# Kernel tuning notes

Hardware: AMD Instinct MI355X
Metric: run time of the kernel (lower is better)

## Reference

```python
import jax, jax.numpy as jnp
import numpy as np

BOARD = 19
TOKENS = BOARD * BOARD          # 361
C = 512
H = 8
DH = C // H                     # 64
MLP = 2048
SPAN = 2 * BOARD - 1            # 37
TABLE = SPAN * SPAN             # 1369
EPS = 1e-6


def _relative_position_index(board_size):
    coords = np.arange(board_size, dtype=np.int32)
    row, col = np.meshgrid(coords, coords, indexing='ij')
    flat = np.stack((row.reshape(-1), col.reshape(-1)), axis=1)
    rel = flat[:, None, :] - flat[None, :, :]
    span = 2 * board_size - 1
    return (rel[..., 0] + board_size - 1) * span + (rel[..., 1] + board_size - 1)


REL_INDEX = jnp.asarray(_relative_position_index(BOARD))  # [T, T] int32


def _layernorm(x, scale, bias):
    mu = jnp.mean(x, axis=-1, keepdims=True)
    var = jnp.mean(jnp.square(x - mu), axis=-1, keepdims=True)
    return (x - mu) * jax.lax.rsqrt(var + EPS) * scale + bias


def setup_inputs() -> dict:
    key = jax.random.key(0)
    ks = jax.random.split(key, 12)
    B = 256
    s = lambda k, shape, sc: jax.random.normal(k, shape, dtype=jnp.float32) * sc
    return {
        'x': s(ks[0], (B, TOKENS, C), 1.0),
        'ln1_scale': jnp.ones((C,), jnp.float32),
        'ln1_bias': jnp.zeros((C,), jnp.float32),
        'Wq': s(ks[1], (C, H, DH), C ** -0.5),
        'bq': jnp.zeros((H, DH), jnp.float32),
        'Wk': s(ks[2], (C, H, DH), C ** -0.5),
        'bk': jnp.zeros((H, DH), jnp.float32),
        'Wv': s(ks[3], (C, H, DH), C ** -0.5),
        'bv': jnp.zeros((H, DH), jnp.float32),
        'Wo': s(ks[4], (C, C), C ** -0.5),
        'bo': jnp.zeros((C,), jnp.float32),
        'rel_pos_bias': s(ks[5], (H, TABLE), 0.02),
        'ln2_scale': jnp.ones((C,), jnp.float32),
        'ln2_bias': jnp.zeros((C,), jnp.float32),
        'W1': s(ks[6], (C, MLP), C ** -0.5),
        'b1': jnp.zeros((MLP,), jnp.float32),
        'W2': s(ks[7], (MLP, C), MLP ** -0.5),
        'b2': jnp.zeros((C,), jnp.float32),
    }


def reference(x, ln1_scale, ln1_bias, Wq, bq, Wk, bk, Wv, bv, Wo, bo,
              rel_pos_bias, ln2_scale, ln2_bias, W1, b1, W2, b2):
    # --- attention ---
    y = _layernorm(x, ln1_scale, ln1_bias)
    q = jnp.einsum('btc,chd->bthd', y, Wq) + bq
    k = jnp.einsum('btc,chd->bthd', y, Wk) + bk
    v = jnp.einsum('btc,chd->bthd', y, Wv) + bv
    logits = jnp.einsum('bthd,bshd->bhts', q, k) * jnp.float32(DH ** -0.5)
    rel_bias = jnp.take(rel_pos_bias, REL_INDEX.reshape(-1), axis=1)
    rel_bias = rel_bias.reshape(H, TOKENS, TOKENS)          # [H, T, T]
    logits = logits + rel_bias[None]
    attn = jax.nn.softmax(logits.astype(jnp.float32), axis=-1).astype(x.dtype)
    ctx = jnp.einsum('bhts,bshd->bthd', attn, v)
    ctx = ctx.reshape(ctx.shape[0], ctx.shape[1], C)
    x = x + ctx @ Wo + bo
    # --- MLP ---
    y = _layernorm(x, ln2_scale, ln2_bias)
    y = jax.nn.gelu(y @ W1 + b1, approximate=True)
    return x + y @ W2 + b2
```

## Files before the change

kernel.cpp:

```cpp
#include <hip/hip_runtime.h>
#include <hip/hip_bf16.h>

#define TOKENS 361
#define CDIM 512
#define NHEAD 8
#define DHEAD 64
#define MLPDIM 2048
#define BATCH 256
#define NTOK (BATCH * TOKENS)
#define HTOK (NTOK / 2)
#define SPAN 37
#define QKVSTR 1536

typedef unsigned int uint32;

typedef __attribute__((ext_vector_type(8))) short bf16x8;
typedef __attribute__((ext_vector_type(4))) float f32x4;

__device__ __forceinline__ unsigned short f2bfu(float f) {
  union { float f; uint32 i; } c; c.f = f;
  uint32 i = c.i;
  uint32 r = (i + 0x7fffu + ((i >> 16) & 1u)) >> 16;
  return (unsigned short)r;
}
__device__ __forceinline__ float bfu2f(unsigned short u) {
  union { uint32 i; float f; } c; c.i = ((uint32)u) << 16; return c.f;
}
__device__ __forceinline__ float lo2f(uint32 u) {
  union { uint32 i; float f; } c; c.i = u << 16; return c.f;
}
__device__ __forceinline__ float hi2f(uint32 u) {
  union { uint32 i; float f; } c; c.i = u & 0xffff0000u; return c.f;
}

__device__ __forceinline__ void gload16(const void* g, void* l) {
  __builtin_amdgcn_global_load_lds((const __attribute__((address_space(1))) void*)g,
                                   (__attribute__((address_space(3))) void*)l, 16, 0, 0);
}

__global__ __launch_bounds__(256) void transpose_conv(
    const float* __restrict__ in, unsigned short* __restrict__ out, int R, int Cc) {
  __shared__ float tile[32][33];
  int c0 = blockIdx.x * 32, r0 = blockIdx.y * 32;
  int tx = threadIdx.x & 31, ty = threadIdx.x >> 5;
#pragma unroll
  for (int i = 0; i < 32; i += 8)
    tile[ty + i][tx] = in[(size_t)(r0 + ty + i) * Cc + c0 + tx];
  __syncthreads();
#pragma unroll
  for (int i = 0; i < 32; i += 8)
    out[(size_t)(c0 + ty + i) * R + r0 + tx] = f2bfu(tile[tx][ty + i]);
}

__global__ __launch_bounds__(256) void concat_bias(
    const float* __restrict__ a, const float* __restrict__ b,
    const float* __restrict__ c, float* __restrict__ o) {
  int i = blockIdx.x * 256 + threadIdx.x;
  o[i] = i < 512 ? a[i] : (i < 1024 ? b[i - 512] : c[i - 1024]);
}

__global__ __launch_bounds__(256) void ln_f32(
    const float* __restrict__ x, const float* __restrict__ sc,
    const float* __restrict__ bs, unsigned short* __restrict__ y) {
  int token = blockIdx.x * 4 + (threadIdx.x >> 6);
  int lane = threadIdx.x & 63;
  const float4* xp = (const float4*)(x + (size_t)token * CDIM + lane * 8);
  float4 f0 = xp[0], f1 = xp[1];
  float v[8] = {f0.x, f0.y, f0.z, f0.w, f1.x, f1.y, f1.z, f1.w};
  float sum = 0.f, sumsq = 0.f;
#pragma unroll
  for (int j = 0; j < 8; ++j) { sum += v[j]; sumsq += v[j] * v[j]; }
#pragma unroll
  for (int off = 1; off < 64; off <<= 1) {
    sum += __shfl_xor(sum, off);
    sumsq += __shfl_xor(sumsq, off);
  }
  float mu = sum * (1.f / 512.f);
  float var = sumsq * (1.f / 512.f) - mu * mu;
  float rs = rsqrtf(var + 1e-6f);
  const float4* sp = (const float4*)(sc + lane * 8);
  const float4* bp = (const float4*)(bs + lane * 8);
  float4 s0 = sp[0], s1 = sp[1], b0 = bp[0], b1 = bp[1];
  float sv[8] = {s0.x, s0.y, s0.z, s0.w, s1.x, s1.y, s1.z, s1.w};
  float bv[8] = {b0.x, b0.y, b0.z, b0.w, b1.x, b1.y, b1.z, b1.w};
  uint32 ov[4];
#pragma unroll
  for (int j = 0; j < 4; ++j) {
    float o0 = (v[2 * j] - mu) * rs * sv[2 * j] + bv[2 * j];
    float o1 = (v[2 * j + 1] - mu) * rs * sv[2 * j + 1] + bv[2 * j + 1];
    ov[j] = (uint32)f2bfu(o0) | ((uint32)f2bfu(o1) << 16);
  }
  uint4 outv = {ov[0], ov[1], ov[2], ov[3]};
  *(uint4*)(y + (size_t)token * CDIM + lane * 8) = outv;
}

__global__ __launch_bounds__(256) void ln_bf16(
    const unsigned short* __restrict__ x, const float* __restrict__ sc,
    const float* __restrict__ bs, unsigned short* __restrict__ y) {
  int token = blockIdx.x * 4 + (threadIdx.x >> 6);
  int lane = threadIdx.x & 63;
  uint4 pk = *(const uint4*)(x + (size_t)token * CDIM + lane * 8);
  uint32 uu[4] = {pk.x, pk.y, pk.z, pk.w};
  float v[8];
#pragma unroll
  for (int j = 0; j < 4; ++j) { v[2 * j] = lo2f(uu[j]); v[2 * j + 1] = hi2f(uu[j]); }
  float sum = 0.f, sumsq = 0.f;
#pragma unroll
  for (int j = 0; j < 8; ++j) { sum += v[j]; sumsq += v[j] * v[j]; }
#pragma unroll
  for (int off = 1; off < 64; off <<= 1) {
    sum += __shfl_xor(sum, off);
    sumsq += __shfl_xor(sumsq, off);
  }
  float mu = sum * (1.f / 512.f);
  float var = sumsq * (1.f / 512.f) - mu * mu;
  float rs = rsqrtf(var + 1e-6f);
  const float4* sp = (const float4*)(sc + lane * 8);
  const float4* bp = (const float4*)(bs + lane * 8);
  float4 s0 = sp[0], s1 = sp[1], b0 = bp[0], b1 = bp[1];
  float sv[8] = {s0.x, s0.y, s0.z, s0.w, s1.x, s1.y, s1.z, s1.w};
  float bv[8] = {b0.x, b0.y, b0.z, b0.w, b1.x, b1.y, b1.z, b1.w};
  uint32 ov[4];
#pragma unroll
  for (int j = 0; j < 4; ++j) {
    float o0 = (v[2 * j] - mu) * rs * sv[2 * j] + bv[2 * j];
    float o1 = (v[2 * j + 1] - mu) * rs * sv[2 * j + 1] + bv[2 * j + 1];
    ov[j] = (uint32)f2bfu(o0) | ((uint32)f2bfu(o1) << 16);
  }
  uint4 outv = {ov[0], ov[1], ov[2], ov[3]};
  *(uint4*)(y + (size_t)token * CDIM + lane * 8) = outv;
}

__device__ __forceinline__ float gelu_tanh(float u) {
  float c2 = 0.7978845608028654f * (u + 0.044715f * u * u * u);
  float e = __expf(2.f * c2);
  float th = 1.f - 2.f / (e + 1.f);
  return 0.5f * u * (1.f + th);
}

template <int EPI>
__global__ __launch_bounds__(256) void gemm_bt(
    const unsigned short* __restrict__ A, const unsigned short* __restrict__ BT,
    const float* __restrict__ bias, const float* __restrict__ resf,
    const unsigned short* __restrict__ resb, void* __restrict__ Cc,
    int M, int N, int K, int nbx) {
  __shared__ unsigned short SH[16384];
  int tid = threadIdx.x;
  int wave = tid >> 6, lane = tid & 63;
  int quad = lane >> 4, l16 = lane & 15;

  int nwg = gridDim.x, bid = blockIdx.x;
  int qq = nwg >> 3, rr = nwg & 7;
  int xcd = bid & 7, loc = bid >> 3;
  int L = (xcd < rr ? xcd * (qq + 1) : rr * (qq + 1) + (xcd - rr) * qq) + loc;
  int m0 = (L / nbx) * 128, n0 = (L % nbx) * 128;
  int wm = (wave >> 1) * 64, wn = (wave & 1) * 64;

  f32x4 acc[4][4];
#pragma unroll
  for (int i = 0; i < 4; ++i)
#pragma unroll
    for (int j = 0; j < 4; ++j) acc[i][j] = (f32x4){0.f, 0.f, 0.f, 0.f};

  int srow = tid >> 2;
  int schunk = ((tid & 3) ^ ((tid >> 3) & 3)) * 8;
  const unsigned short* gA = A + (size_t)(m0 + srow) * K + schunk;
  const unsigned short* gA2 = gA + (size_t)64 * K;
  const unsigned short* gB = BT + (size_t)(n0 + srow) * K + schunk;
  const unsigned short* gB2 = gB + (size_t)64 * K;

  {
    unsigned short* a = SH;
    unsigned short* bS = SH + 8192;
    gload16(gA, a + wave * 512);
    gload16(gA2, a + 2048 + wave * 512);
    gload16(gB, bS + wave * 512);
    gload16(gB2, bS + 2048 + wave * 512);
  }
  __syncthreads();

  int rq = (quad ^ ((l16 >> 1) & 3)) * 8;
  int cur = 0;
  for (int k0 = 0; k0 < K; k0 += 32) {
    if (k0 + 32 < K) {
      int nb = cur ^ 1;
      unsigned short* a = SH + nb * 4096;
      unsigned short* bS = SH + 8192 + nb * 4096;
      gload16(gA + k0 + 32, a + wave * 512);
      gload16(gA2 + k0 + 32, a + 2048 + wave * 512);
      gload16(gB + k0 + 32, bS + wave * 512);
      gload16(gB2 + k0 + 32, bS + 2048 + wave * 512);
    }
    const unsigned short* As = SH + cur * 4096;
    const unsigned short* Bs = SH + 8192 + cur * 4096;
    bf16x8 af[4], bfr[4];
#pragma unroll
    for (int mi = 0; mi < 4; ++mi)
      af[mi] = *(const bf16x8*)&As[(wm + mi * 16 + l16) * 32 + rq];
#pragma unroll
    for (int ni = 0; ni < 4; ++ni)
      bfr[ni] = *(const bf16x8*)&Bs[(wn + ni * 16 + l16) * 32 + rq];
#pragma unroll
    for (int mi = 0; mi < 4; ++mi)
#pragma unroll
      for (int ni = 0; ni < 4; ++ni)
        acc[mi][ni] = __builtin_amdgcn_mfma_f32_16x16x32_bf16(af[mi], bfr[ni], acc[mi][ni], 0, 0, 0);
    __syncthreads();
    cur ^= 1;
  }

  unsigned short* o16 = (unsigned short*)Cc;
  float* o32 = (float*)Cc;
  if (EPI == 3) {
#pragma unroll
    for (int ni = 0; ni < 4; ++ni) {
      int gc = n0 + wn + ni * 16 + l16;
      float bz = bias[gc];
#pragma unroll
      for (int mi = 0; mi < 4; ++mi) {
#pragma unroll
        for (int r = 0; r < 4; ++r) {
          int gr = m0 + wm + mi * 16 + quad * 4 + r;
          float val = acc[mi][ni][r] + bz;
          val += bfu2f(resb[(size_t)gr * N + gc]);
          o32[(size_t)gr * N + gc] = val;
        }
      }
    }
  } else {
#pragma unroll
    for (int ni = 0; ni < 4; ++ni) {
      int gc = n0 + wn + ni * 16 + l16;
      float bz = bias[gc];
#pragma unroll
      for (int mi = 0; mi < 4; ++mi) {
#pragma unroll
        for (int r = 0; r < 4; ++r) {
          int lr = wm + mi * 16 + quad * 4 + r;
          float val = acc[mi][ni][r] + bz;
          if (EPI == 1) val = gelu_tanh(val);
          if (EPI == 2) val += resf[(size_t)(m0 + lr) * N + gc];
          SH[lr * 128 + wn + ni * 16 + l16] = f2bfu(val);
        }
      }
    }
    __syncthreads();
    int tg = tid >> 4, t15 = tid & 15;
#pragma unroll
    for (int j = 0; j < 8; ++j) {
      int row = j * 16 + tg;
      uint4 w = *(const uint4*)&SH[row * 128 + t15 * 8];
      *(uint4*)(o16 + (size_t)(m0 + row) * N + n0 + t15 * 8) = w;
    }
  }
}

#define SROW 72
#define PSTR 392
__global__ __launch_bounds__(256, 1) void attn_mfma(
    const unsigned short* __restrict__ qkv, const float* __restrict__ relb,
    unsigned short* __restrict__ ctx) {
  __shared__ unsigned short Ks[368 * SROW];
  __shared__ unsigned short VT[64 * PSTR];
  __shared__ unsigned short Ps[64 * PSTR];
  __shared__ float biasF[1369];
  int b = blockIdx.x >> 3, h = blockIdx.x & 7;
  int tid = threadIdx.x;
  int wave = tid >> 6, lane = tid & 63;
  int quad = lane >> 4, l16 = lane & 15;
  size_t baseq = ((size_t)b * TOKENS) * QKVSTR + h * DHEAD;
  size_t basec = ((size_t)b * TOKENS) * CDIM + h * DHEAD;
  const unsigned short* kp = qkv + baseq + 512;
  const unsigned short* vp = qkv + baseq + 1024;

  for (int vv = tid; vv < TOKENS * 8; vv += 256) {
    int r = vv >> 3, c = (vv & 7) * 8;
    *(uint4*)&Ks[r * SROW + c] = *(const uint4*)(kp + (size_t)r * QKVSTR + c);
  }
  if (tid < 56) {
    int r = 361 + (tid >> 3), c = (tid & 7) * 8;
    *(uint4*)&Ks[r * SROW + c] = (uint4){0u, 0u, 0u, 0u};
  }
  for (int vv = tid; vv < TOKENS * 8; vv += 256) {
    int s = vv >> 3, c = (vv & 7) * 8;
    uint4 pk = *(const uint4*)(vp + (size_t)s * QKVSTR + c);
    unsigned short* dst = &VT[c * PSTR + s];
    uint32 w0 = pk.x, w1 = pk.y, w2 = pk.z, w3 = pk.w;
    dst[0]        = (unsigned short)w0;  dst[PSTR]     = (unsigned short)(w0 >> 16);
    dst[2 * PSTR] = (unsigned short)w1;  dst[3 * PSTR] = (unsigned short)(w1 >> 16);
    dst[4 * PSTR] = (unsigned short)w2;  dst[5 * PSTR] = (unsigned short)(w2 >> 16);
    dst[6 * PSTR] = (unsigned short)w3;  dst[7 * PSTR] = (unsigned short)(w3 >> 16);
  }
  for (int vv = tid; vv < 64 * 23; vv += 256) {
    int s = 361 + (vv >> 6), d = vv & 63;
    VT[d * PSTR + s] = 0;
  }
  for (int i = tid; i < 1369; i += 256) biasF[i] = relb[h * 1369 + i];
  for (int i = lane; i < 256; i += 64) {
    int rrp = i >> 4, cc = i & 15;
    Ps[(wave * 16 + rrp) * PSTR + 368 + cc] = 0;
  }
  __syncthreads();

  for (int t0 = 0; t0 < TOKENS; t0 += 64) {
    int rowb = t0 + wave * 16;
    const unsigned short* qrow = qkv + baseq + (size_t)(rowb + l16) * QKVSTR + quad * 8;
    bf16x8 aq0 = *(const bf16x8*)(qrow);
    bf16x8 aq1 = *(const bf16x8*)(qrow + 32);
    int tb[4];
#pragma unroll
    for (int r = 0; r < 4; ++r) {
      int t = rowb + quad * 4 + r;
      if (t > 360) t = 360;
      int rt = t / 19, ct = t - rt * 19;
      tb[r] = rt * SPAN + ct + (18 * SPAN + 18);
    }
    f32x4 sc[23];
#pragma unroll
    for (int n = 0; n < 23; ++n) {
      const unsigned short* kr = &Ks[(n * 16 + l16) * SROW + quad * 8];
      bf16x8 b0 = *(const bf16x8*)kr;
      bf16x8 b1 = *(const bf16x8*)(kr + 32);
      f32x4 a = {0.f, 0.f, 0.f, 0.f};
      a = __builtin_amdgcn_mfma_f32_16x16x32_bf16(aq0, b0, a, 0, 0, 0);
      a = __builtin_amdgcn_mfma_f32_16x16x32_bf16(aq1, b1, a, 0, 0, 0);
      sc[n] = a;
    }
    float mx[4] = {-1e30f, -1e30f, -1e30f, -1e30f};
#pragma unroll
    for (int n = 0; n < 23; ++n) {
      int s = n * 16 + l16;
      int sv = s > 360 ? 360 : s;
      int rs = sv / 19, cs = sv - rs * 19;
      int sb = rs * SPAN + cs;
#pragma unroll
      for (int r = 0; r < 4; ++r) {
        float val = sc[n][r] * 0.125f + biasF[tb[r] - sb];
        if (s > 360) val = -1e30f;
        sc[n][r] = val;
        mx[r] = fmaxf(mx[r], val);
      }
    }
#pragma unroll
    for (int off = 1; off < 16; off <<= 1)
#pragma unroll
      for (int r = 0; r < 4; ++r) mx[r] = fmaxf(mx[r], __shfl_xor(mx[r], off));
    float sm[4] = {0.f, 0.f, 0.f, 0.f};
#pragma unroll
    for (int n = 0; n < 23; ++n)
#pragma unroll
      for (int r = 0; r < 4; ++r) {
        float p = __expf(sc[n][r] - mx[r]);
        sc[n][r] = p;
        sm[r] += p;
      }
#pragma unroll
    for (int off = 1; off < 16; off <<= 1)
#pragma unroll
      for (int r = 0; r < 4; ++r) sm[r] += __shfl_xor(sm[r], off);
    float inv[4];
#pragma unroll
    for (int r = 0; r < 4; ++r) inv[r] = 1.f / sm[r];
#pragma unroll
    for (int n = 0; n < 23; ++n)
#pragma unroll
      for (int r = 0; r < 4; ++r)
        Ps[(wave * 16 + quad * 4 + r) * PSTR + n * 16 + l16] = f2bfu(sc[n][r] * inv[r]);
    f32x4 pacc[4];
#pragma unroll
    for (int ni = 0; ni < 4; ++ni) pacc[ni] = (f32x4){0.f, 0.f, 0.f, 0.f};
#pragma unroll
    for (int kk = 0; kk < 12; ++kk) {
      bf16x8 pa = *(const bf16x8*)&Ps[(wave * 16 + l16) * PSTR + kk * 32 + quad * 8];
#pragma unroll
      for (int ni = 0; ni < 4; ++ni) {
        bf16x8 vb = *(const bf16x8*)&VT[(ni * 16 + l16) * PSTR + kk * 32 + quad * 8];
        pacc[ni] = __builtin_amdgcn_mfma_f32_16x16x32_bf16(pa, vb, pacc[ni], 0, 0, 0);
      }
    }
#pragma unroll
    for (int ni = 0; ni < 4; ++ni)
#pragma unroll
      for (int r = 0; r < 4; ++r) {
        int t = rowb + quad * 4 + r;
        if (t < TOKENS)
          ctx[basec + (size_t)t * CDIM + ni * 16 + l16] = f2bfu(pacc[ni][r]);
      }
  }
}

extern "C" void kernel_launch(void* const* d_in, const int* in_sizes, int n_in,
                              void* d_out, int out_size, void* d_ws, size_t ws_size,
                              hipStream_t stream) {
  const float* x     = (const float*)d_in[0];
  const float* ln1_s = (const float*)d_in[1];
  const float* ln1_b = (const float*)d_in[2];
  const float* Wq    = (const float*)d_in[3];
  const float* bq    = (const float*)d_in[4];
  const float* Wk    = (const float*)d_in[5];
  const float* bk    = (const float*)d_in[6];
  const float* Wv    = (const float*)d_in[7];
  const float* bv    = (const float*)d_in[8];
  const float* Wo    = (const float*)d_in[9];
  const float* bo    = (const float*)d_in[10];
  const float* relb  = (const float*)d_in[11];
  const float* ln2_s = (const float*)d_in[12];
  const float* ln2_b = (const float*)d_in[13];
  const float* W1    = (const float*)d_in[14];
  const float* b1    = (const float*)d_in[15];
  const float* W2    = (const float*)d_in[16];
  const float* b2    = (const float*)d_in[17];
  float* out = (float*)d_out;

  char* ws = (char*)d_ws;
  unsigned short* WqT = (unsigned short*)ws;
  unsigned short* WkT = WqT + 512 * 512;
  unsigned short* WvT = WkT + 512 * 512;
  unsigned short* WoT = WvT + 512 * 512;
  unsigned short* W1T = WoT + 512 * 512;
  unsigned short* W2T = W1T + 512 * 2048;
  float* bqkv = (float*)(W2T + 2048 * 512);
  unsigned short* yb  = (unsigned short*)(bqkv + 1536);
  unsigned short* x1b = yb + (size_t)NTOK * CDIM;
  unsigned short* qkvb = x1b + (size_t)NTOK * CDIM;
  unsigned short* ctxb = qkvb + (size_t)HTOK * QKVSTR;
  unsigned short* hdn  = qkvb;

  dim3 blk(256);
  transpose_conv<<<dim3(16, 16), blk, 0, stream>>>(Wq, WqT, 512, 512);
  transpose_conv<<<dim3(16, 16), blk, 0, stream>>>(Wk, WkT, 512, 512);
  transpose_conv<<<dim3(16, 16), blk, 0, stream>>>(Wv, WvT, 512, 512);
  transpose_conv<<<dim3(16, 16), blk, 0, stream>>>(Wo, WoT, 512, 512);
  transpose_conv<<<dim3(64, 16), blk, 0, stream>>>(W1, W1T, 512, 2048);
  transpose_conv<<<dim3(16, 64), blk, 0, stream>>>(W2, W2T, 2048, 512);
  concat_bias<<<dim3(6), blk, 0, stream>>>(bq, bk, bv, bqkv);

  ln_f32<<<NTOK / 4, blk, 0, stream>>>(x, ln1_s, ln1_b, yb);

  for (int c = 0; c < 2; ++c) {
    size_t off = (size_t)c * HTOK;
    const unsigned short* yc = yb + off * CDIM;
    gemm_bt<0><<<dim3(361 * 12), blk, 0, stream>>>(yc, WqT, bqkv, nullptr, nullptr,
                                                   qkvb, HTOK, 1536, 512, 12);
    attn_mfma<<<dim3((BATCH / 2) * NHEAD), blk, 0, stream>>>(qkvb, relb, ctxb);
    gemm_bt<2><<<dim3(361 * 4), blk, 0, stream>>>(ctxb, WoT, bo, x + off * CDIM, nullptr,
                                                  x1b + off * CDIM, HTOK, 512, 512, 4);
  }

  ln_bf16<<<NTOK / 4, blk, 0, stream>>>(x1b, ln2_s, ln2_b, yb);

  for (int c = 0; c < 2; ++c) {
    size_t off = (size_t)c * HTOK;
    gemm_bt<1><<<dim3(361 * 16), blk, 0, stream>>>(yb + off * CDIM, W1T, b1, nullptr, nullptr,
                                                   hdn, HTOK, 2048, 512, 16);
    gemm_bt<3><<<dim3(361 * 4), blk, 0, stream>>>(hdn, W2T, b2, nullptr, x1b + off * CDIM,
                                                  out + off * CDIM, HTOK, 512, 2048, 4);
  }
}
```

Before: 1.717 ms.

## Swizzle attention LDS layouts, widen to 8 waves, stage EPI3 epilogue through LDS

The attention kernel now runs 512 threads (8 waves), so each block covers 128 query rows per iteration, three iterations in total. K, V-transpose and P are stored in LDS with XOR swizzles instead of padded strides, which is meant to avoid bank conflicts. P is written and consumed in three chunks so the LDS buffer for it is smaller, and s_setprio is raised around the MFMA loops. Separately, the fp32 residual epilogue of the GEMM is staged through shared memory in two halves so the residual reads and fp32 output writes become vectorized and coalesced. The cost is extra barriers in that epilogue and more register pressure in the wider attention block.

```diff
diff --git a/kernel.cpp b/kernel.cpp
--- a/kernel.cpp
+++ b/kernel.cpp
@@ -212,19 +212,35 @@
   unsigned short* o16 = (unsigned short*)Cc;
   float* o32 = (float*)Cc;
   if (EPI == 3) {
-#pragma unroll
-    for (int ni = 0; ni < 4; ++ni) {
-      int gc = n0 + wn + ni * 16 + l16;
-      float bz = bias[gc];
-#pragma unroll
-      for (int mi = 0; mi < 4; ++mi) {
-#pragma unroll
-        for (int r = 0; r < 4; ++r) {
-          int gr = m0 + wm + mi * 16 + quad * 4 + r;
-          float val = acc[mi][ni][r] + bz;
-          val += bfu2f(resb[(size_t)gr * N + gc]);
-          o32[(size_t)gr * N + gc] = val;
+    float* SHf = (float*)SH;
+#pragma unroll
+    for (int h2 = 0; h2 < 2; ++h2) {
+      __syncthreads();
+      if ((wn >> 6) == h2) {
+#pragma unroll
+        for (int ni = 0; ni < 4; ++ni) {
+          float bz = bias[n0 + h2 * 64 + ni * 16 + l16];
+#pragma unroll
+          for (int mi = 0; mi < 4; ++mi) {
+#pragma unroll
+            for (int r = 0; r < 4; ++r) {
+              int row = wm + mi * 16 + quad * 4 + r;
+              SHf[row * 64 + ni * 16 + l16] = acc[mi][ni][r] + bz;
+            }
+          }
         }
+      }
+      __syncthreads();
+#pragma unroll
+      for (int j = 0; j < 8; ++j) {
+        int idx = j * 256 + tid;
+        int row = idx >> 4, c4 = (idx & 15) * 4;
+        size_t goff = (size_t)(m0 + row) * N + n0 + h2 * 64 + c4;
+        uint2 rb = *(const uint2*)(resb + goff);
+        float4 sv = *(const float4*)&SHf[row * 64 + c4];
+        sv.x += lo2f(rb.x); sv.y += hi2f(rb.x);
+        sv.z += lo2f(rb.y); sv.w += hi2f(rb.y);
+        *(float4*)(o32 + goff) = sv;
       }
     }
   } else {
@@ -255,55 +271,53 @@
   }
 }
 
-#define SROW 72
-#define PSTR 392
-__global__ __launch_bounds__(256, 1) void attn_mfma(
+#define KROW 64
+#define VROW 384
+#define PROW 128
+__global__ __launch_bounds__(512, 1) void attn_mfma(
     const unsigned short* __restrict__ qkv, const float* __restrict__ relb,
     unsigned short* __restrict__ ctx) {
-  __shared__ unsigned short Ks[368 * SROW];
-  __shared__ unsigned short VT[64 * PSTR];
-  __shared__ unsigned short Ps[64 * PSTR];
+  __shared__ unsigned short Ks[384 * KROW];
+  __shared__ unsigned short VT[64 * VROW];
+  __shared__ unsigned short Ps[128 * PROW];
   __shared__ float biasF[1369];
   int b = blockIdx.x >> 3, h = blockIdx.x & 7;
   int tid = threadIdx.x;
   int wave = tid >> 6, lane = tid & 63;
   int quad = lane >> 4, l16 = lane & 15;
+  int l8 = l16 & 7;
   size_t baseq = ((size_t)b * TOKENS) * QKVSTR + h * DHEAD;
   size_t basec = ((size_t)b * TOKENS) * CDIM + h * DHEAD;
   const unsigned short* kp = qkv + baseq + 512;
   const unsigned short* vp = qkv + baseq + 1024;
 
-  for (int vv = tid; vv < TOKENS * 8; vv += 256) {
-    int r = vv >> 3, c = (vv & 7) * 8;
-    *(uint4*)&Ks[r * SROW + c] = *(const uint4*)(kp + (size_t)r * QKVSTR + c);
-  }
-  if (tid < 56) {
-    int r = 361 + (tid >> 3), c = (tid & 7) * 8;
-    *(uint4*)&Ks[r * SROW + c] = (uint4){0u, 0u, 0u, 0u};
-  }
-  for (int vv = tid; vv < TOKENS * 8; vv += 256) {
+  for (int vv = tid; vv < 384 * 8; vv += 512) {
+    int r = vv >> 3, c8 = vv & 7;
+    uint4 val = (uint4){0u, 0u, 0u, 0u};
+    if (r < TOKENS) val = *(const uint4*)(kp + (size_t)r * QKVSTR + c8 * 8);
+    *(uint4*)&Ks[r * KROW + ((c8 ^ (r & 7)) << 3)] = val;
+  }
+  for (int vv = tid; vv < TOKENS * 8; vv += 512) {
     int s = vv >> 3, c = (vv & 7) * 8;
     uint4 pk = *(const uint4*)(vp + (size_t)s * QKVSTR + c);
-    unsigned short* dst = &VT[c * PSTR + s];
-    uint32 w0 = pk.x, w1 = pk.y, w2 = pk.z, w3 = pk.w;
-    dst[0]        = (unsigned short)w0;  dst[PSTR]     = (unsigned short)(w0 >> 16);
-    dst[2 * PSTR] = (unsigned short)w1;  dst[3 * PSTR] = (unsigned short)(w1 >> 16);
-    dst[4 * PSTR] = (unsigned short)w2;  dst[5 * PSTR] = (unsigned short)(w2 >> 16);
-    dst[6 * PSTR] = (unsigned short)w3;  dst[7 * PSTR] = (unsigned short)(w3 >> 16);
-  }
-  for (int vv = tid; vv < 64 * 23; vv += 256) {
+    uint32 w[4] = {pk.x, pk.y, pk.z, pk.w};
+    int g0 = s >> 3, s7 = s & 7;
+#pragma unroll
+    for (int j = 0; j < 8; ++j) {
+      unsigned short hv = (unsigned short)(w[j >> 1] >> ((j & 1) * 16));
+      int d0 = c + j;
+      VT[d0 * VROW + ((g0 ^ (d0 & 7)) << 3) + s7] = hv;
+    }
+  }
+  for (int vv = tid; vv < 64 * 23; vv += 512) {
     int s = 361 + (vv >> 6), d = vv & 63;
-    VT[d * PSTR + s] = 0;
-  }
-  for (int i = tid; i < 1369; i += 256) biasF[i] = relb[h * 1369 + i];
-  for (int i = lane; i < 256; i += 64) {
-    int rrp = i >> 4, cc = i & 15;
-    Ps[(wave * 16 + rrp) * PSTR + 368 + cc] = 0;
-  }
+    VT[d * VROW + (((s >> 3) ^ (d & 7)) << 3) + (s & 7)] = 0;
+  }
+  for (int i = tid; i < 1369; i += 512) biasF[i] = relb[h * 1369 + i];
   __syncthreads();
 
-  for (int t0 = 0; t0 < TOKENS; t0 += 64) {
-    int rowb = t0 + wave * 16;
+  for (int it = 0; it < 3; ++it) {
+    int rowb = it * 128 + wave * 16;
     const unsigned short* qrow = qkv + baseq + (size_t)(rowb + l16) * QKVSTR + quad * 8;
     bf16x8 aq0 = *(const bf16x8*)(qrow);
     bf16x8 aq1 = *(const bf16x8*)(qrow + 32);
@@ -315,20 +329,22 @@
       int rt = t / 19, ct = t - rt * 19;
       tb[r] = rt * SPAN + ct + (18 * SPAN + 18);
     }
-    f32x4 sc[23];
-#pragma unroll
-    for (int n = 0; n < 23; ++n) {
-      const unsigned short* kr = &Ks[(n * 16 + l16) * SROW + quad * 8];
-      bf16x8 b0 = *(const bf16x8*)kr;
-      bf16x8 b1 = *(const bf16x8*)(kr + 32);
+    f32x4 sc[24];
+    __builtin_amdgcn_s_setprio(1);
+#pragma unroll
+    for (int n = 0; n < 24; ++n) {
+      const unsigned short* kr = &Ks[(n * 16 + l16) * KROW];
+      bf16x8 b0 = *(const bf16x8*)(kr + ((quad ^ l8) << 3));
+      bf16x8 b1 = *(const bf16x8*)(kr + (((quad + 4) ^ l8) << 3));
       f32x4 a = {0.f, 0.f, 0.f, 0.f};
       a = __builtin_amdgcn_mfma_f32_16x16x32_bf16(aq0, b0, a, 0, 0, 0);
       a = __builtin_amdgcn_mfma_f32_16x16x32_bf16(aq1, b1, a, 0, 0, 0);
       sc[n] = a;
     }
+    __builtin_amdgcn_s_setprio(0);
     float mx[4] = {-1e30f, -1e30f, -1e30f, -1e30f};
 #pragma unroll
-    for (int n = 0; n < 23; ++n) {
+    for (int n = 0; n < 24; ++n) {
       int s = n * 16 + l16;
       int sv = s > 360 ? 360 : s;
       int rs = sv / 19, cs = sv - rs * 19;
@@ -347,7 +363,7 @@
       for (int r = 0; r < 4; ++r) mx[r] = fmaxf(mx[r], __shfl_xor(mx[r], off));
     float sm[4] = {0.f, 0.f, 0.f, 0.f};
 #pragma unroll
-    for (int n = 0; n < 23; ++n)
+    for (int n = 0; n < 24; ++n)
 #pragma unroll
       for (int r = 0; r < 4; ++r) {
         float p = __expf(sc[n][r] - mx[r]);
@@ -361,22 +377,34 @@
     float inv[4];
 #pragma unroll
     for (int r = 0; r < 4; ++r) inv[r] = 1.f / sm[r];
-#pragma unroll
-    for (int n = 0; n < 23; ++n)
-#pragma unroll
-      for (int r = 0; r < 4; ++r)
-        Ps[(wave * 16 + quad * 4 + r) * PSTR + n * 16 + l16] = f2bfu(sc[n][r] * inv[r]);
     f32x4 pacc[4];
 #pragma unroll
     for (int ni = 0; ni < 4; ++ni) pacc[ni] = (f32x4){0.f, 0.f, 0.f, 0.f};
 #pragma unroll
-    for (int kk = 0; kk < 12; ++kk) {
-      bf16x8 pa = *(const bf16x8*)&Ps[(wave * 16 + l16) * PSTR + kk * 32 + quad * 8];
-#pragma unroll
-      for (int ni = 0; ni < 4; ++ni) {
-        bf16x8 vb = *(const bf16x8*)&VT[(ni * 16 + l16) * PSTR + kk * 32 + quad * 8];
-        pacc[ni] = __builtin_amdgcn_mfma_f32_16x16x32_bf16(pa, vb, pacc[ni], 0, 0, 0);
-      }
+    for (int ch = 0; ch < 3; ++ch) {
+#pragma unroll
+      for (int nl = 0; nl < 8; ++nl) {
+        int n = ch * 8 + nl;
+#pragma unroll
+        for (int r = 0; r < 4; ++r) {
+          int prow = wave * 16 + quad * 4 + r;
+          int g = ((nl << 1) + (l16 >> 3)) ^ ((quad * 4 + r) & 7);
+          Ps[prow * PROW + (g << 3) + l8] = f2bfu(sc[n][r] * inv[r]);
+        }
+      }
+      __builtin_amdgcn_s_setprio(1);
+#pragma unroll
+      for (int kk = 0; kk < 4; ++kk) {
+        bf16x8 pa = *(const bf16x8*)&Ps[(wave * 16 + l16) * PROW +
+                                        ((((kk << 2) + quad) ^ l8) << 3)];
+#pragma unroll
+        for (int ni = 0; ni < 4; ++ni) {
+          bf16x8 vb = *(const bf16x8*)&VT[(ni * 16 + l16) * VROW +
+                                          ((((ch << 4) + (kk << 2) + quad) ^ l8) << 3)];
+          pacc[ni] = __builtin_amdgcn_mfma_f32_16x16x32_bf16(pa, vb, pacc[ni], 0, 0, 0);
+        }
+      }
+      __builtin_amdgcn_s_setprio(0);
     }
 #pragma unroll
     for (int ni = 0; ni < 4; ++ni)
@@ -442,7 +470,7 @@
     const unsigned short* yc = yb + off * CDIM;
     gemm_bt<0><<<dim3(361 * 12), blk, 0, stream>>>(yc, WqT, bqkv, nullptr, nullptr,
                                                    qkvb, HTOK, 1536, 512, 12);
-    attn_mfma<<<dim3((BATCH / 2) * NHEAD), blk, 0, stream>>>(qkvb, relb, ctxb);
+    attn_mfma<<<dim3((BATCH / 2) * NHEAD), dim3(512), 0, stream>>>(qkvb, relb, ctxb);
     gemm_bt<2><<<dim3(361 * 4), blk, 0, stream>>>(ctxb, WoT, bo, x + off * CDIM, nullptr,
                                                   x1b + off * CDIM, HTOK, 512, 512, 4);
   }
```

Measured after the change: 1.557 ms. 1.1x faster.
